# Kernel optimization log

Measured on AMD Instinct MI355X. Metric: run time of the kernel, lower is better.

Reference implementation:

```python
import jax, jax.numpy as jnp
import numpy as np

HEAD_NUM = 16
MASK_FILL = 100000.0  # source uses +1e5 on masked entries (not -inf)


def setup_inputs() -> dict:
    key = jax.random.key(0)
    k1, k2, k3, k4, k5 = jax.random.split(key, 5)
    B, S, E = 2, 2048, 1024
    scale = 0.02
    return {
        "x": jax.random.normal(k1, (B, S, E), dtype=jnp.float32),
        "W_atten": jax.random.normal(k2, (E, 3 * E), dtype=jnp.float32) * scale,
        "b_atten": jax.random.normal(k3, (3 * E,), dtype=jnp.float32) * scale,
        "W_proj": jax.random.normal(k4, (E, E), dtype=jnp.float32) * scale,
        "b_proj": jax.random.normal(k5, (E,), dtype=jnp.float32) * scale,
    }


def reference(x, W_atten, b_atten, W_proj, b_proj):
    B, S, E = x.shape
    H = HEAD_NUM
    hd = E // H
    # QKV projection: [B, S, 3E]
    qkv = x @ W_atten + b_atten
    # reshape [B, S, H, 3*hd] -> [B, H, S, 3*hd], chunk into q,k,v [B,H,S,hd]
    qkv = jnp.transpose(qkv.reshape(B, S, H, 3 * hd), (0, 2, 1, 3))
    q, k, v = jnp.split(qkv, 3, axis=-1)
    # raw scores, NO 1/sqrt(dk) scaling (faithful to source)
    w = jnp.einsum("bhqd,bhkd->bhqk", q, k)
    # causal mask applied as w*mask + (1-mask)*1e5 (faithful to source)
    mask = jnp.tril(jnp.ones((S, S), dtype=w.dtype))
    w = w * mask + (1.0 - mask) * MASK_FILL
    # softmax over dim=1 == HEAD axis (faithful to source quirk)
    w = jax.nn.softmax(w, axis=1)
    # attn_drop: identity in eval mode
    a = jnp.einsum("bhqk,bhkd->bhqd", w, v)  # [B,H,S,hd]
    a = jnp.transpose(a, (0, 2, 1, 3)).reshape(B, S, E)
    h = a @ W_proj + b_proj
    # resi_drop: identity in eval mode
    return h
```

## Files before the change

kernel.cpp:

```cpp
#include <hip/hip_runtime.h>

#define DI __device__ __forceinline__

typedef __attribute__((ext_vector_type(8))) short s16x8;
typedef __attribute__((ext_vector_type(4))) short s16x4;
typedef __attribute__((ext_vector_type(4))) float f32x4;

DI unsigned short f2bf(float f){
  unsigned u = __float_as_uint(f);
  u = (u + 0x7FFFu + ((u >> 16) & 1u)) >> 16;
  return (unsigned short)u;
}
DI float bf2f(unsigned short h){
  return __uint_as_float(((unsigned)h) << 16);
}
DI float exp2i(float x){ float r; asm("v_exp_f32 %0, %1" : "=v"(r) : "v"(x)); return r; }

DI void gll16(const void* g, void* l){
  __builtin_amdgcn_global_load_lds((const __attribute__((address_space(1))) void*)g,
                                   (__attribute__((address_space(3))) void*)l, 16, 0, 0);
}

#define VMCNT(n) asm volatile("s_waitcnt vmcnt(" #n ")" ::: "memory")

__global__ void cvt_kernel(const float* __restrict__ in, unsigned short* __restrict__ out, int n8){
  int i = blockIdx.x * blockDim.x + threadIdx.x;
  if (i >= n8) return;
  const float4* p = (const float4*)in + (size_t)i * 2;
  float4 a = p[0], b = p[1];
  s16x8 o;
  o[0] = (short)f2bf(a.x); o[1] = (short)f2bf(a.y); o[2] = (short)f2bf(a.z); o[3] = (short)f2bf(a.w);
  o[4] = (short)f2bf(b.x); o[5] = (short)f2bf(b.y); o[6] = (short)f2bf(b.z); o[7] = (short)f2bf(b.w);
  ((s16x8*)out)[i] = o;
}

__global__ void transpose_cvt(const float* __restrict__ in, unsigned short* __restrict__ out, int R, int C){
  __shared__ float t[32][33];
  int c0 = blockIdx.x * 32, r0 = blockIdx.y * 32;
  int tx = threadIdx.x, ty = threadIdx.y;
  #pragma unroll
  for (int i = 0; i < 4; i++)
    t[ty + i*8][tx] = in[(size_t)(r0 + ty + i*8) * C + c0 + tx];
  __syncthreads();
  #pragma unroll
  for (int i = 0; i < 4; i++)
    out[(size_t)(c0 + ty + i*8) * R + r0 + tx] = f2bf(t[tx][ty + i*8]);
}

template<int MODE, int BM>
__launch_bounds__(256)
__global__ void gemm_kernel(const unsigned short* __restrict__ A,
                            const unsigned short* __restrict__ Wt,
                            const float* __restrict__ bias,
                            int N,
                            unsigned short* __restrict__ qb,
                            unsigned short* __restrict__ kb,
                            unsigned short* __restrict__ vt,
                            float* __restrict__ out)
{
  constexpr int MI = BM / 32;
  constexpr int AC = BM / 32;
  const int K = 1024;
  __shared__ unsigned short As[BM * 64];
  __shared__ unsigned short Bs[128 * 64];
  int m0 = blockIdx.y * BM, n0 = blockIdx.x * 128;
  int tid = threadIdx.x;
  int lane = tid & 63, w = tid >> 6;
  int row_l = lane & 15, kgrp = lane >> 4;
  int wm = (w >> 1) * (MI * 16), wn = (w & 1) * 64;

  const unsigned short* asrc[AC];
  const unsigned short* bsrc[4];
  int ldsoA[AC], ldsoB[4];
  int chunk = (lane & 7) ^ (lane >> 3);
  #pragma unroll
  for (int c4 = 0; c4 < AC; c4++){
    int r = c4*32 + w*8 + (lane >> 3);
    asrc[c4] = A + (size_t)(m0 + r) * K + chunk*8;
    ldsoA[c4] = (c4*32 + w*8) * 64;
  }
  #pragma unroll
  for (int c4 = 0; c4 < 4; c4++){
    int r = c4*32 + w*8 + (lane >> 3);
    bsrc[c4] = Wt + (size_t)(n0 + r) * K + chunk*8;
    ldsoB[c4] = (c4*32 + w*8) * 64;
  }
  int eA[MI], eB[4];
  #pragma unroll
  for (int i = 0; i < MI; i++){
    int ra = wm + i*16 + row_l;
    eA[i] = (ra*64 + kgrp*8) ^ ((ra & 7) << 3);
  }
  #pragma unroll
  for (int i = 0; i < 4; i++){
    int rb = wn + i*16 + row_l;
    eB[i] = (rb*64 + kgrp*8) ^ ((rb & 7) << 3);
  }

  f32x4 acc[MI][4];
  #pragma unroll
  for (int i = 0; i < MI; i++)
    #pragma unroll
    for (int j = 0; j < 4; j++)
      acc[i][j] = (f32x4){0.f, 0.f, 0.f, 0.f};

  for (int k0 = 0; k0 < K; k0 += 64){
    #pragma unroll
    for (int c4 = 0; c4 < AC; c4++)
      gll16(asrc[c4] + k0, (void*)(As + ldsoA[c4]));
    #pragma unroll
    for (int c4 = 0; c4 < 4; c4++)
      gll16(bsrc[c4] + k0, (void*)(Bs + ldsoB[c4]));
    __syncthreads();
    #pragma unroll
    for (int kc = 0; kc < 2; kc++){
      s16x8 af[MI], bfr[4];
      #pragma unroll
      for (int mi = 0; mi < MI; mi++)
        af[mi] = *(const s16x8*)&As[eA[mi] ^ (kc*32)];
      #pragma unroll
      for (int ni = 0; ni < 4; ni++)
        bfr[ni] = *(const s16x8*)&Bs[eB[ni] ^ (kc*32)];
      #pragma unroll
      for (int mi = 0; mi < MI; mi++)
        #pragma unroll
        for (int ni = 0; ni < 4; ni++)
          acc[mi][ni] = __builtin_amdgcn_mfma_f32_16x16x32_bf16(af[mi], bfr[ni], acc[mi][ni], 0, 0, 0);
    }
    __syncthreads();
  }

  #pragma unroll
  for (int mi = 0; mi < MI; mi++){
    #pragma unroll
    for (int ni = 0; ni < 4; ni++){
      #pragma unroll
      for (int j = 0; j < 4; j++){
        int gr = m0 + wm + mi*16 + kgrp*4 + j;
        int gc = n0 + wn + ni*16 + row_l;
        float v = acc[mi][ni][j] + bias[gc];
        if (MODE == 0){
          int h = gc / 192, cc = gc % 192;
          int b = gr >> 11, s = gr & 2047;
          if (cc < 64){
            qb[(size_t)gr * 1024 + h*64 + cc] = f2bf(v * 1.44269504f);
          } else if (cc < 128){
            int d = cc - 64; int kt = s >> 6, kk = s & 63;
            kb[(size_t)((b*16 + h)*32 + kt) * 4096 + ((kk*64 + d) ^ ((kk & 7) << 3))] = f2bf(v);
          } else {
            int d = cc - 128; int kt = s >> 6, kk = s & 63;
            vt[(size_t)((b*16 + h)*32 + kt) * 4096 + ((d*64 + kk) ^ ((d & 7) << 3))] = f2bf(v);
          }
        } else {
          out[(size_t)gr * N + gc] = v;
        }
      }
    }
  }
}

__global__ void sufv_kernel(const unsigned short* __restrict__ vt, float* __restrict__ sufv){
  __shared__ float tot[4][64];
  int bh = blockIdx.x;
  int tid = threadIdx.x;
  int tq = tid >> 6, d = tid & 63;
  const unsigned short* base = vt + (size_t)bh * 32 * 4096;
  float s[8];
  float run = 0.f;
  for (int j = 7; j >= 0; j--){
    int t = tq*8 + j;
    float rs = 0.f;
    #pragma unroll
    for (int c = 0; c < 8; c++){
      int idx = (d*64 + c*8) ^ ((d & 7) << 3);
      s16x8 v = *(const s16x8*)&base[(size_t)t*4096 + idx];
      #pragma unroll
      for (int e = 0; e < 8; e++) rs += bf2f((unsigned short)v[e]);
    }
    run += rs; s[j] = run;
  }
  tot[tq][d] = run;
  __syncthreads();
  float carry = 0.f;
  for (int t2 = tq+1; t2 < 4; t2++) carry += tot[t2][d];
  #pragma unroll
  for (int j = 0; j < 8; j++)
    sufv[((size_t)bh*33 + tq*8 + j)*64 + d] = s[j] + carry;
  if (tid < 64) sufv[((size_t)bh*33 + 32)*64 + tid] = 0.f;
}

__launch_bounds__(256)
__global__ void dpass_kernel(const unsigned short* __restrict__ qbuf,
                             const unsigned short* __restrict__ kb,
                             unsigned short* __restrict__ invb)
{
  __shared__ unsigned short Kst[4][4096];
  int bid = blockIdx.x;
  int blk = (bid & 7) * 132 + (bid >> 3);
  int b = blk / 528, t = blk % 528;
  int kt = (int)(32.5f - sqrtf(1056.25f - 2.f*t));
  while (kt*(65-kt)/2 > t) kt--;
  while ((kt+1)*(64-kt)/2 <= t) kt++;
  int qt = kt + (t - kt*(65-kt)/2);

  int tid = threadIdx.x, lane = tid & 63, w = tid >> 6;
  int row_l = lane & 15, kgrp = lane >> 4;

  const unsigned short* ktb = kb + ((size_t)(b*16)*32 + kt) * 4096;
  int sgoff = (w*128 + lane)*8;

  auto stage = [&](int hh, int buf){
    const unsigned short* src = ktb + (size_t)hh * 131072;
    gll16(src + sgoff,       (void*)(&Kst[buf][0] + w*1024));
    gll16(src + sgoff + 512, (void*)(&Kst[buf][0] + w*1024 + 512));
  };

  int e0[4];
  #pragma unroll
  for (int ks = 0; ks < 4; ks++){
    int row = ks*16 + row_l;
    e0[ks] = (row*64 + kgrp*8) ^ ((row & 7) << 3);
  }

  stage(0, 0);
  stage(1, 1);

  f32x4 esum[4];
  #pragma unroll
  for (int ks = 0; ks < 4; ks++) esum[ks] = (f32x4){0.f,0.f,0.f,0.f};

  const unsigned short* qrow_p = qbuf + (size_t)(b*2048 + qt*64 + w*16 + row_l) * 1024;
  s16x8 qf0 = *(const s16x8*)&qrow_p[kgrp*8];
  s16x8 qf1 = *(const s16x8*)&qrow_p[32 + kgrp*8];

  for (int h = 0; h < 16; h++){
    s16x8 qn0, qn1;
    if (h < 15){
      qn0 = *(const s16x8*)&qrow_p[(h+1)*64 + kgrp*8];
      qn1 = *(const s16x8*)&qrow_p[(h+1)*64 + 32 + kgrp*8];
    }
    if (h + 2 < 16) stage(h+2, (h+2) & 3);
    __builtin_amdgcn_sched_barrier(0);
    if (h < 14)      VMCNT(8);
    else if (h < 15) VMCNT(6);
    else             VMCNT(2);
    __builtin_amdgcn_sched_barrier(0);
    __builtin_amdgcn_s_barrier();
    __builtin_amdgcn_sched_barrier(0);

    const unsigned short* kl = &Kst[h & 3][0];
    #pragma unroll
    for (int ks = 0; ks < 4; ks++){
      s16x8 a0 = *(const s16x8*)&kl[e0[ks]];
      s16x8 a1 = *(const s16x8*)&kl[e0[ks] ^ 32];
      f32x4 sc = __builtin_amdgcn_mfma_f32_16x16x32_bf16(a0, qf0, (f32x4){0.f,0.f,0.f,0.f}, 0, 0, 0);
      sc = __builtin_amdgcn_mfma_f32_16x16x32_bf16(a1, qf1, sc, 0, 0, 0);
      #pragma unroll
      for (int j = 0; j < 4; j++) esum[ks][j] += exp2i(sc[j]);
    }
    if (h < 15){ qf0 = qn0; qf1 = qn1; }
  }

  int qcol = qt*64 + w*16 + row_l;
  unsigned short* dst = invb + (size_t)b*4194304 + (size_t)qcol*2048 + kt*64 + kgrp*4;
  #pragma unroll
  for (int ks = 0; ks < 4; ks++){
    float r0 = 1.f/esum[ks][0], r1 = 1.f/esum[ks][1];
    float r2 = 1.f/esum[ks][2], r3 = 1.f/esum[ks][3];
    unsigned lo, hi;
    asm("v_cvt_pk_bf16_f32 %0, %1, %2" : "=v"(lo) : "v"(r0), "v"(r1));
    asm("v_cvt_pk_bf16_f32 %0, %1, %2" : "=v"(hi) : "v"(r2), "v"(r3));
    uint2 pk; pk.x = lo; pk.y = hi;
    *(uint2*)&dst[ks*16] = pk;
  }
}

__launch_bounds__(256, 3)
__global__ void pv_kernel(const unsigned short* __restrict__ qbuf,
                          const unsigned short* __restrict__ kb,
                          const unsigned short* __restrict__ vt,
                          const unsigned short* __restrict__ invb,
                          const float* __restrict__ sufv,
                          unsigned short* __restrict__ ab,
                          float* __restrict__ pb)
{
  __shared__ unsigned short Kst[3][4096];
  __shared__ unsigned short Vst[2][4096];
  __shared__ unsigned short Wsh[4][1152];

  int blk = ((blockIdx.x & 7) << 7) + (blockIdx.x >> 3);
  int b = blk >> 9;
  int r = blk & 511;
  int h = r >> 5;
  int r2 = r & 31;
  int i = r2 >> 1, half = r2 & 1;
  int qsm = i, qbig = 31 - i;

  int tid = threadIdx.x, lane = tid & 63, w = tid >> 6;
  int row_l = lane & 15, kgrp = lane >> 4;

  const unsigned short* KT = kb + (size_t)((b*16 + h)*32) * 4096;
  const unsigned short* VT = vt + (size_t)((b*16 + h)*32) * 4096;
  int sgoff = (w*128 + lane)*8;
  unsigned short* Wsw = &Wsh[w][0];

  int eK[4];
  #pragma unroll
  for (int ks = 0; ks < 4; ks++){
    int row = ks*16 + row_l;
    eK[ks] = (row*64 + kgrp*8) ^ ((row & 7) << 3);
  }

  auto stageK = [&](int kt, int buf){
    gll16(KT + (size_t)kt*4096 + sgoff,       (void*)(&Kst[buf][0] + w*1024));
    gll16(KT + (size_t)kt*4096 + sgoff + 512, (void*)(&Kst[buf][0] + w*1024 + 512));
  };
  auto stageV = [&](int kt, int buf){
    gll16(VT + (size_t)kt*4096 + sgoff,       (void*)(&Vst[buf][0] + w*1024));
    gll16(VT + (size_t)kt*4096 + sgoff + 512, (void*)(&Vst[buf][0] + w*1024 + 512));
  };

  auto run = [&](int qt, int k0t, int k1t, int mode){
    int q0 = qt * 64;
    int qv = q0 + w*16 + row_l;
    const unsigned short* qrow_p = qbuf + (size_t)(b*2048 + qv) * 1024 + h*64;
    s16x8 qf0 = *(const s16x8*)&qrow_p[kgrp*8];
    s16x8 qf1 = *(const s16x8*)&qrow_p[32 + kgrp*8];
    const unsigned short* ivrow = invb + (size_t)b*4194304 + (size_t)qv*2048 + kgrp*4;

    f32x4 pvv[4];
    #pragma unroll
    for (int d = 0; d < 4; d++) pvv[d] = (f32x4){0.f,0.f,0.f,0.f};

    __syncthreads();
    stageK(k0t, 0);
    s16x4 i1[4], i2[4];
    #pragma unroll
    for (int ks = 0; ks < 4; ks++) i1[ks] = *(const s16x4*)&ivrow[k0t*64 + ks*16];
    stageV(k0t, 0);
    if (k0t + 1 < k1t){
      stageK(k0t+1, 1);
      #pragma unroll
      for (int ks = 0; ks < 4; ks++) i2[ks] = *(const s16x4*)&ivrow[(k0t+1)*64 + ks*16];
    }

    for (int kt = k0t; kt < k1t; kt++){
      int bK = (kt - k0t) % 3, bV = (kt - k0t) & 1;
      bool nx1 = (kt + 1 < k1t), nx2 = (kt + 2 < k1t);

      __builtin_amdgcn_s_barrier();
      if (nx2) stageK(kt+2, (kt+2-k0t) % 3);
      if (nx1) stageV(kt+1, bV ^ 1);
      __builtin_amdgcn_sched_barrier(0);
      int N = (kt == k0t) ? (nx1 ? (nx2 ? 10 : 8) : 0)
                          : (nx2 ? 8 : (nx1 ? 6 : 0));
      if (N == 10)     VMCNT(10);
      else if (N == 8) VMCNT(8);
      else if (N == 6) VMCNT(6);
      else             VMCNT(0);
      __builtin_amdgcn_sched_barrier(0);
      __builtin_amdgcn_s_barrier();
      __builtin_amdgcn_sched_barrier(0);

      s16x4 icur[4];
      #pragma unroll
      for (int ks = 0; ks < 4; ks++){ icur[ks] = i1[ks]; i1[ks] = i2[ks]; }
      if (nx2){
        #pragma unroll
        for (int ks = 0; ks < 4; ks++) i2[ks] = *(const s16x4*)&ivrow[(kt+2)*64 + ks*16];
      }

      const unsigned short* kl = &Kst[bK][0];
      const unsigned short* vl = &Vst[bV][0];
      f32x4 sc[4];
      __builtin_amdgcn_s_setprio(1);
      #pragma unroll
      for (int ks = 0; ks < 4; ks++){
        s16x8 a0 = *(const s16x8*)&kl[eK[ks]];
        s16x8 a1 = *(const s16x8*)&kl[eK[ks] ^ 32];
        sc[ks] = __builtin_amdgcn_mfma_f32_16x16x32_bf16(a0, qf0, (f32x4){0.f,0.f,0.f,0.f}, 0, 0, 0);
        sc[ks] = __builtin_amdgcn_mfma_f32_16x16x32_bf16(a1, qf1, sc[ks], 0, 0, 0);
      }
      __builtin_amdgcn_s_setprio(0);

      if (kt == qt){
        int kbase = kt*64 + kgrp*4;
        #pragma unroll
        for (int ks = 0; ks < 4; ks++){
          #pragma unroll
          for (int j = 0; j < 4; j++){
            float wv = exp2i(sc[ks][j]) * bf2f((unsigned short)icur[ks][j]);
            sc[ks][j] = (kbase + ks*16 + j > qv) ? 0.0625f : wv;
          }
          unsigned lo, hi;
          asm("v_cvt_pk_bf16_f32 %0, %1, %2" : "=v"(lo) : "v"(sc[ks][0]), "v"(sc[ks][1]));
          asm("v_cvt_pk_bf16_f32 %0, %1, %2" : "=v"(hi) : "v"(sc[ks][2]), "v"(sc[ks][3]));
          uint2 pk2; pk2.x = lo; pk2.y = hi;
          *(uint2*)&Wsw[row_l*72 + ks*16 + kgrp*4] = pk2;
        }
      } else {
        #pragma unroll
        for (int ks = 0; ks < 4; ks++){
          #pragma unroll
          for (int j = 0; j < 4; j++)
            sc[ks][j] = exp2i(sc[ks][j]) * bf2f((unsigned short)icur[ks][j]);
          unsigned lo, hi;
          asm("v_cvt_pk_bf16_f32 %0, %1, %2" : "=v"(lo) : "v"(sc[ks][0]), "v"(sc[ks][1]));
          asm("v_cvt_pk_bf16_f32 %0, %1, %2" : "=v"(hi) : "v"(sc[ks][2]), "v"(sc[ks][3]));
          uint2 pk2; pk2.x = lo; pk2.y = hi;
          *(uint2*)&Wsw[row_l*72 + ks*16 + kgrp*4] = pk2;
        }
      }

      __builtin_amdgcn_s_setprio(1);
      #pragma unroll
      for (int kc = 0; kc < 2; kc++){
        s16x8 af = *(const s16x8*)&Wsw[row_l*72 + kc*32 + kgrp*8];
        #pragma unroll
        for (int dq = 0; dq < 4; dq++){
          s16x8 vf = *(const s16x8*)&vl[eK[dq] ^ (kc*32)];
          pvv[dq] = __builtin_amdgcn_mfma_f32_16x16x32_bf16(af, vf, pvv[dq], 0, 0, 0);
        }
      }
      __builtin_amdgcn_s_setprio(0);
    }

    if (mode == 0){
      int tsuf = qt + 1;
      #pragma unroll
      for (int dq = 0; dq < 4; dq++){
        int d = dq*16 + row_l;
        float suf = sufv[((size_t)(b*16 + h)*33 + tsuf)*64 + d];
        #pragma unroll
        for (int j = 0; j < 4; j++){
          int qo = q0 + w*16 + kgrp*4 + j;
          ab[(size_t)(b*2048 + qo)*1024 + h*64 + d] = f2bf(pvv[dq][j] + 0.0625f * suf);
        }
      }
    } else {
      float* pr = pb + ((size_t)((b*16 + h)*16 + i)*2 + (mode - 1)) * 4096;
      #pragma unroll
      for (int dq = 0; dq < 4; dq++){
        int d = dq*16 + row_l;
        #pragma unroll
        for (int j = 0; j < 4; j++)
          pr[(w*16 + kgrp*4 + j)*64 + d] = pvv[dq][j];
      }
    }
  };

  if (half == 0){
    run(qsm, 0, i + 1, 0);
    run(qbig, 0, 16 - i, 1);
  } else {
    run(qbig, 16 - i, 32 - i, 2);
  }
}

__global__ void reduce_kernel(const float* __restrict__ pb,
                              const float* __restrict__ sufv,
                              unsigned short* __restrict__ ab)
{
  int blk = blockIdx.x;
  int b = blk >> 8, rr = blk & 255;
  int h = rr >> 4, i = rr & 15;
  int qbig = 31 - i, tsuf = 32 - i;
  int t = threadIdx.x;
  int q = t >> 2, dbase = (t & 3) * 16;
  const float* p0 = pb + ((size_t)((b*16 + h)*16 + i)*2 + 0)*4096 + q*64 + dbase;
  const float* p1 = p0 + 4096;
  const float* sf = sufv + ((size_t)(b*16 + h)*33 + tsuf)*64 + dbase;
  unsigned short* op = ab + (size_t)(b*2048 + qbig*64 + q)*1024 + h*64 + dbase;
  #pragma unroll
  for (int e = 0; e < 4; e++){
    float4 a = *(const float4*)(p0 + e*4);
    float4 bb = *(const float4*)(p1 + e*4);
    float4 s = *(const float4*)(sf + e*4);
    unsigned short o[4];
    o[0] = f2bf(a.x + bb.x + 0.0625f * s.x);
    o[1] = f2bf(a.y + bb.y + 0.0625f * s.y);
    o[2] = f2bf(a.z + bb.z + 0.0625f * s.z);
    o[3] = f2bf(a.w + bb.w + 0.0625f * s.w);
    *(s16x4*)(op + e*4) = *(s16x4*)o;
  }
}

extern "C" void kernel_launch(void* const* d_in, const int* in_sizes, int n_in,
                              void* d_out, int out_size, void* d_ws, size_t ws_size,
                              hipStream_t stream) {
  (void)in_sizes; (void)n_in; (void)out_size; (void)ws_size;
  const float* x  = (const float*)d_in[0];
  const float* Wa = (const float*)d_in[1];
  const float* ba = (const float*)d_in[2];
  const float* Wp = (const float*)d_in[3];
  const float* bp = (const float*)d_in[4];
  float* out = (float*)d_out;

  char* ws = (char*)d_ws;
  size_t off = 0;
  auto alloc = [&](size_t bytes) -> void* {
    void* p = ws + off;
    off += (bytes + 255) & ~(size_t)255;
    return p;
  };
  float* pbuf          = (float*)alloc((size_t)16*1024*1024);
  unsigned short* xb   = (unsigned short*)((char*)pbuf);
  unsigned short* WaT  = (unsigned short*)((char*)pbuf + (size_t)4096*1024*2);
  unsigned short* WpT  = (unsigned short*)alloc((size_t)1024*1024*2);
  unsigned short* qbuf = (unsigned short*)alloc((size_t)4096*1024*2);
  unsigned short* ktile= (unsigned short*)alloc((size_t)4096*1024*2);
  unsigned short* vtile= (unsigned short*)alloc((size_t)4096*1024*2);
  unsigned short* abuf = (unsigned short*)alloc((size_t)4096*1024*2);
  unsigned short* invb = (unsigned short*)alloc((size_t)2*2048*2048*2);
  float* sufv          = (float*)alloc((size_t)32*33*64*4);

  cvt_kernel<<<2048, 256, 0, stream>>>(x, xb, 4096*1024/8);
  transpose_cvt<<<dim3(3072/32, 1024/32), dim3(32, 8), 0, stream>>>(Wa, WaT, 1024, 3072);
  transpose_cvt<<<dim3(1024/32, 1024/32), dim3(32, 8), 0, stream>>>(Wp, WpT, 1024, 1024);

  gemm_kernel<0,128><<<dim3(24, 32), 256, 0, stream>>>(xb, WaT, ba, 3072, qbuf, ktile, vtile, nullptr);

  sufv_kernel<<<32, 256, 0, stream>>>(vtile, sufv);

  dpass_kernel<<<1056, 256, 0, stream>>>(qbuf, ktile, invb);

  pv_kernel<<<1024, 256, 0, stream>>>(qbuf, ktile, vtile, invb, sufv, abuf, pbuf);

  reduce_kernel<<<512, 256, 0, stream>>>(pbuf, sufv, abuf);

  gemm_kernel<1,64><<<dim3(1024/128, 4096/64), 256, 0, stream>>>(abuf, WpT, bp, 1024, nullptr, nullptr, nullptr, out);
}
```

Baseline: 178.7 us.

## Split pv_kernel into single-wave blocks with direct V register loads

Restructures pv_kernel from 256-thread blocks, where four waves share staged K/V tiles, into 4096 single-wave blocks. Each wave stages its own K tile into LDS with double buffering and loads V fragments straight from global memory into registers. This removes block-level barriers and the shared V staging. The cost is that K and V are each fetched four times more, since waves no longer share tiles, and global V loads are uncoalesced under the swizzled index.

```diff
diff --git a/kernel.cpp b/kernel.cpp
--- a/kernel.cpp
+++ b/kernel.cpp
@@ -275,7 +275,7 @@
   }
 }
 
-__launch_bounds__(256, 3)
+__launch_bounds__(64)
 __global__ void pv_kernel(const unsigned short* __restrict__ qbuf,
                           const unsigned short* __restrict__ kb,
                           const unsigned short* __restrict__ vt,
@@ -284,40 +284,34 @@
                           unsigned short* __restrict__ ab,
                           float* __restrict__ pb)
 {
-  __shared__ unsigned short Kst[3][4096];
-  __shared__ unsigned short Vst[2][4096];
-  __shared__ unsigned short Wsh[4][1152];
-
-  int blk = ((blockIdx.x & 7) << 7) + (blockIdx.x >> 3);
-  int b = blk >> 9;
-  int r = blk & 511;
-  int h = r >> 5;
-  int r2 = r & 31;
-  int i = r2 >> 1, half = r2 & 1;
+  __shared__ unsigned short Kst[2][4096];
+  __shared__ unsigned short Wsh[16 * 72];
+
+  int bid = blockIdx.x;
+  int blk = ((bid & 7) << 9) | (bid >> 3);
+  int w    = blk & 3;
+  int half = (blk >> 2) & 1;
+  int i    = (blk >> 3) & 15;
+  int h    = (blk >> 7) & 15;
+  int b    = blk >> 11;
   int qsm = i, qbig = 31 - i;
 
-  int tid = threadIdx.x, lane = tid & 63, w = tid >> 6;
+  int lane = threadIdx.x & 63;
   int row_l = lane & 15, kgrp = lane >> 4;
 
   const unsigned short* KT = kb + (size_t)((b*16 + h)*32) * 4096;
   const unsigned short* VT = vt + (size_t)((b*16 + h)*32) * 4096;
-  int sgoff = (w*128 + lane)*8;
-  unsigned short* Wsw = &Wsh[w][0];
 
   int eK[4];
   #pragma unroll
-  for (int ks = 0; ks < 4; ks++){
-    int row = ks*16 + row_l;
-    eK[ks] = (row*64 + kgrp*8) ^ ((row & 7) << 3);
-  }
+  for (int ks = 0; ks < 4; ks++)
+    eK[ks] = ((ks*16 + row_l)*64 + kgrp*8) ^ ((row_l & 7) << 3);
 
   auto stageK = [&](int kt, int buf){
-    gll16(KT + (size_t)kt*4096 + sgoff,       (void*)(&Kst[buf][0] + w*1024));
-    gll16(KT + (size_t)kt*4096 + sgoff + 512, (void*)(&Kst[buf][0] + w*1024 + 512));
-  };
-  auto stageV = [&](int kt, int buf){
-    gll16(VT + (size_t)kt*4096 + sgoff,       (void*)(&Vst[buf][0] + w*1024));
-    gll16(VT + (size_t)kt*4096 + sgoff + 512, (void*)(&Vst[buf][0] + w*1024 + 512));
+    const unsigned short* src = KT + (size_t)kt*4096 + lane*8;
+    #pragma unroll
+    for (int c = 0; c < 8; c++)
+      gll16(src + c*512, (void*)(&Kst[buf][0] + c*512 + lane*8));
   };
 
   auto run = [&](int qt, int k0t, int k1t, int mode){
@@ -332,46 +326,36 @@
     #pragma unroll
     for (int d = 0; d < 4; d++) pvv[d] = (f32x4){0.f,0.f,0.f,0.f};
 
-    __syncthreads();
     stageK(k0t, 0);
-    s16x4 i1[4], i2[4];
+    s16x4 i1[4];
     #pragma unroll
     for (int ks = 0; ks < 4; ks++) i1[ks] = *(const s16x4*)&ivrow[k0t*64 + ks*16];
-    stageV(k0t, 0);
-    if (k0t + 1 < k1t){
-      stageK(k0t+1, 1);
-      #pragma unroll
-      for (int ks = 0; ks < 4; ks++) i2[ks] = *(const s16x4*)&ivrow[(k0t+1)*64 + ks*16];
-    }
 
     for (int kt = k0t; kt < k1t; kt++){
-      int bK = (kt - k0t) % 3, bV = (kt - k0t) & 1;
-      bool nx1 = (kt + 1 < k1t), nx2 = (kt + 2 < k1t);
-
-      __builtin_amdgcn_s_barrier();
-      if (nx2) stageK(kt+2, (kt+2-k0t) % 3);
-      if (nx1) stageV(kt+1, bV ^ 1);
+      int buf = (kt - k0t) & 1;
+      bool nx = (kt + 1 < k1t);
+
+      const unsigned short* vp = VT + (size_t)kt*4096;
+      s16x8 vr[8];
+      #pragma unroll
+      for (int kc = 0; kc < 2; kc++)
+        #pragma unroll
+        for (int dq = 0; dq < 4; dq++)
+          vr[kc*4+dq] = *(const s16x8*)&vp[eK[dq] ^ (kc*32)];
+      if (nx) stageK(kt+1, buf ^ 1);
+      s16x4 icur[4];
+      #pragma unroll
+      for (int ks = 0; ks < 4; ks++) icur[ks] = i1[ks];
+      if (nx){
+        #pragma unroll
+        for (int ks = 0; ks < 4; ks++) i1[ks] = *(const s16x4*)&ivrow[(kt+1)*64 + ks*16];
+      }
       __builtin_amdgcn_sched_barrier(0);
-      int N = (kt == k0t) ? (nx1 ? (nx2 ? 10 : 8) : 0)
-                          : (nx2 ? 8 : (nx1 ? 6 : 0));
-      if (N == 10)     VMCNT(10);
-      else if (N == 8) VMCNT(8);
-      else if (N == 6) VMCNT(6);
-      else             VMCNT(0);
+      if (nx) VMCNT(24);
+      else    VMCNT(12);
       __builtin_amdgcn_sched_barrier(0);
-      __builtin_amdgcn_s_barrier();
-      __builtin_amdgcn_sched_barrier(0);
-
-      s16x4 icur[4];
-      #pragma unroll
-      for (int ks = 0; ks < 4; ks++){ icur[ks] = i1[ks]; i1[ks] = i2[ks]; }
-      if (nx2){
-        #pragma unroll
-        for (int ks = 0; ks < 4; ks++) i2[ks] = *(const s16x4*)&ivrow[(kt+2)*64 + ks*16];
-      }
-
-      const unsigned short* kl = &Kst[bK][0];
-      const unsigned short* vl = &Vst[bV][0];
+
+      const unsigned short* kl = &Kst[buf][0];
       f32x4 sc[4];
       __builtin_amdgcn_s_setprio(1);
       #pragma unroll
@@ -396,7 +380,7 @@
           asm("v_cvt_pk_bf16_f32 %0, %1, %2" : "=v"(lo) : "v"(sc[ks][0]), "v"(sc[ks][1]));
           asm("v_cvt_pk_bf16_f32 %0, %1, %2" : "=v"(hi) : "v"(sc[ks][2]), "v"(sc[ks][3]));
           uint2 pk2; pk2.x = lo; pk2.y = hi;
-          *(uint2*)&Wsw[row_l*72 + ks*16 + kgrp*4] = pk2;
+          *(uint2*)&Wsh[row_l*72 + ks*16 + kgrp*4] = pk2;
         }
       } else {
         #pragma unroll
@@ -408,19 +392,17 @@
           asm("v_cvt_pk_bf16_f32 %0, %1, %2" : "=v"(lo) : "v"(sc[ks][0]), "v"(sc[ks][1]));
           asm("v_cvt_pk_bf16_f32 %0, %1, %2" : "=v"(hi) : "v"(sc[ks][2]), "v"(sc[ks][3]));
           uint2 pk2; pk2.x = lo; pk2.y = hi;
-          *(uint2*)&Wsw[row_l*72 + ks*16 + kgrp*4] = pk2;
+          *(uint2*)&Wsh[row_l*72 + ks*16 + kgrp*4] = pk2;
         }
       }
 
       __builtin_amdgcn_s_setprio(1);
       #pragma unroll
       for (int kc = 0; kc < 2; kc++){
-        s16x8 af = *(const s16x8*)&Wsw[row_l*72 + kc*32 + kgrp*8];
-        #pragma unroll
-        for (int dq = 0; dq < 4; dq++){
-          s16x8 vf = *(const s16x8*)&vl[eK[dq] ^ (kc*32)];
-          pvv[dq] = __builtin_amdgcn_mfma_f32_16x16x32_bf16(af, vf, pvv[dq], 0, 0, 0);
-        }
+        s16x8 af = *(const s16x8*)&Wsh[row_l*72 + kc*32 + kgrp*8];
+        #pragma unroll
+        for (int dq = 0; dq < 4; dq++)
+          pvv[dq] = __builtin_amdgcn_mfma_f32_16x16x32_bf16(af, vr[kc*4+dq], pvv[dq], 0, 0, 0);
       }
       __builtin_amdgcn_s_setprio(0);
     }
@@ -524,7 +506,7 @@
 
   dpass_kernel<<<1056, 256, 0, stream>>>(qbuf, ktile, invb);
 
-  pv_kernel<<<1024, 256, 0, stream>>>(qbuf, ktile, vtile, invb, sufv, abuf, pbuf);
+  pv_kernel<<<4096, 64, 0, stream>>>(qbuf, ktile, vtile, invb, sufv, abuf, pbuf);
 
   reduce_kernel<<<512, 256, 0, stream>>>(pbuf, sufv, abuf);
 
```

Result: slower. 198.9 us (+11.3%).

## Restructure pv_kernel pipeline to single barrier per tile with 4-deep K ring

Applied to the files above, without the earlier changes.

Expands the K staging ring from three to four buffers indexed by absolute tile, which lets the loop drop the leading barrier. V staging now goes after the barrier. The prefetch of the inverse-sum scalars is shortened from two tiles ahead to one, and the vmcnt thresholds are re-derived to match. It also removes the setprio hints and relaxes launch_bounds from 3 to default waves per SIMD. Extra LDS (8 KB more per block) may reduce occupancy, and the new ordering relies on the vmcnt counts being correct.

```diff
diff --git a/kernel.cpp b/kernel.cpp
--- a/kernel.cpp
+++ b/kernel.cpp
@@ -275,7 +275,7 @@
   }
 }
 
-__launch_bounds__(256, 3)
+__launch_bounds__(256)
 __global__ void pv_kernel(const unsigned short* __restrict__ qbuf,
                           const unsigned short* __restrict__ kb,
                           const unsigned short* __restrict__ vt,
@@ -284,7 +284,7 @@
                           unsigned short* __restrict__ ab,
                           float* __restrict__ pb)
 {
-  __shared__ unsigned short Kst[3][4096];
+  __shared__ unsigned short Kst[4][4096];
   __shared__ unsigned short Vst[2][4096];
   __shared__ unsigned short Wsh[4][1152];
 
@@ -333,47 +333,45 @@
     for (int d = 0; d < 4; d++) pvv[d] = (f32x4){0.f,0.f,0.f,0.f};
 
     __syncthreads();
-    stageK(k0t, 0);
-    s16x4 i1[4], i2[4];
+    stageK(k0t, k0t & 3);
+    stageV(k0t, k0t & 1);
+    s16x4 i1[4];
     #pragma unroll
     for (int ks = 0; ks < 4; ks++) i1[ks] = *(const s16x4*)&ivrow[k0t*64 + ks*16];
-    stageV(k0t, 0);
-    if (k0t + 1 < k1t){
-      stageK(k0t+1, 1);
-      #pragma unroll
-      for (int ks = 0; ks < 4; ks++) i2[ks] = *(const s16x4*)&ivrow[(k0t+1)*64 + ks*16];
-    }
+    if (k0t + 1 < k1t) stageK(k0t+1, (k0t+1) & 3);
 
     for (int kt = k0t; kt < k1t; kt++){
-      int bK = (kt - k0t) % 3, bV = (kt - k0t) & 1;
       bool nx1 = (kt + 1 < k1t), nx2 = (kt + 2 < k1t);
-
-      __builtin_amdgcn_s_barrier();
-      if (nx2) stageK(kt+2, (kt+2-k0t) % 3);
-      if (nx1) stageV(kt+1, bV ^ 1);
+      bool first = (kt == k0t);
+
+      s16x4 icur[4];
+      #pragma unroll
+      for (int ks = 0; ks < 4; ks++) icur[ks] = i1[ks];
+      if (nx1){
+        #pragma unroll
+        for (int ks = 0; ks < 4; ks++) i1[ks] = *(const s16x4*)&ivrow[(kt+1)*64 + ks*16];
+      }
+      if (nx2) stageK(kt+2, (kt+2) & 3);
+
       __builtin_amdgcn_sched_barrier(0);
-      int N = (kt == k0t) ? (nx1 ? (nx2 ? 10 : 8) : 0)
-                          : (nx2 ? 8 : (nx1 ? 6 : 0));
-      if (N == 10)     VMCNT(10);
-      else if (N == 8) VMCNT(8);
-      else if (N == 6) VMCNT(6);
-      else             VMCNT(0);
+      if (first){
+        if (nx2)      VMCNT(12);
+        else if (nx1) VMCNT(10);
+        else          VMCNT(4);
+      } else {
+        if (nx2)      VMCNT(6);
+        else if (nx1) VMCNT(4);
+        else          VMCNT(0);
+      }
       __builtin_amdgcn_sched_barrier(0);
       __builtin_amdgcn_s_barrier();
       __builtin_amdgcn_sched_barrier(0);
 
-      s16x4 icur[4];
-      #pragma unroll
-      for (int ks = 0; ks < 4; ks++){ icur[ks] = i1[ks]; i1[ks] = i2[ks]; }
-      if (nx2){
-        #pragma unroll
-        for (int ks = 0; ks < 4; ks++) i2[ks] = *(const s16x4*)&ivrow[(kt+2)*64 + ks*16];
-      }
-
-      const unsigned short* kl = &Kst[bK][0];
-      const unsigned short* vl = &Vst[bV][0];
+      if (nx1) stageV(kt+1, (kt+1) & 1);
+
+      const unsigned short* kl = &Kst[kt & 3][0];
+      const unsigned short* vl = &Vst[kt & 1][0];
       f32x4 sc[4];
-      __builtin_amdgcn_s_setprio(1);
       #pragma unroll
       for (int ks = 0; ks < 4; ks++){
         s16x8 a0 = *(const s16x8*)&kl[eK[ks]];
@@ -381,7 +379,6 @@
         sc[ks] = __builtin_amdgcn_mfma_f32_16x16x32_bf16(a0, qf0, (f32x4){0.f,0.f,0.f,0.f}, 0, 0, 0);
         sc[ks] = __builtin_amdgcn_mfma_f32_16x16x32_bf16(a1, qf1, sc[ks], 0, 0, 0);
       }
-      __builtin_amdgcn_s_setprio(0);
 
       if (kt == qt){
         int kbase = kt*64 + kgrp*4;
@@ -412,7 +409,6 @@
         }
       }
 
-      __builtin_amdgcn_s_setprio(1);
       #pragma unroll
       for (int kc = 0; kc < 2; kc++){
         s16x8 af = *(const s16x8*)&Wsw[row_l*72 + kc*32 + kgrp*8];
@@ -422,7 +418,6 @@
           pvv[dq] = __builtin_amdgcn_mfma_f32_16x16x32_bf16(af, vf, pvv[dq], 0, 0, 0);
         }
       }
-      __builtin_amdgcn_s_setprio(0);
     }
 
     if (mode == 0){
```

Measured after the change: 180.6 us. About the same (+1.1%).
